# Kernel optimization log

Hardware: AMD Instinct MI355X
Metric: run time of the kernel (lower is better)

Reference implementation:

```python
import math
import jax, jax.numpy as jnp
import numpy as np

BLOCK = 128
QMAX = 7.0            # 2**(4-1) - 1
ALPHA = 2.5139        # optimal Gaussian scale for 4 bits
N_LEVELS = 2 * 7 + 1  # 15
TRUST = ALPHA / N_LEVELS


def _build_hadamard(size: int) -> np.ndarray:
    H = np.ones((1, 1), dtype=np.float64)
    while H.shape[0] < size:
        H = np.block([[H, H], [H, -H]])
    return (H / math.sqrt(size)).astype(np.float32)


def _hadamard_rotate(x, H):
    # blockwise rotation along last dim; H is symmetric orthogonal so this is
    # its own inverse
    *batch, dim = x.shape
    bs = H.shape[0]
    return (x.reshape(*batch, dim // bs, bs) @ H).reshape(*batch, dim)


def setup_inputs() -> dict:
    key = jax.random.key(0)
    x = jax.random.normal(key, (4, 4096, 4096), dtype=jnp.float32)
    H = jnp.asarray(_build_hadamard(BLOCK))
    return {"x": x, "H": H}


def reference(x, H):
    x_h = _hadamard_rotate(x, H)
    # RMS over last dim
    std = jnp.maximum(jnp.sqrt(jnp.mean(x_h * x_h, axis=-1, keepdims=True)), 1e-8)
    step = (ALPHA * std) / QMAX
    xq = jnp.clip(jnp.round(x_h / step), -QMAX, QMAX) * step
    mask = (jnp.abs(xq - x_h) <= std * TRUST).astype(x_h.dtype)
    # straight-through: gradient flows only through x_h * mask
    out_h = x_h * mask + jax.lax.stop_gradient(xq - x_h * mask)
    return _hadamard_rotate(out_h, H)
```

## Files before the change

kernel.cpp:

```cpp
#include <hip/hip_runtime.h>
#include <hip/hip_bf16.h>


#define HTQ_ALPHA 2.5139f
#define HTQ_QMAX  7.0f

template <int CTRL>
__device__ __forceinline__ float dpp_perm(float f) {
    int r = __builtin_amdgcn_update_dpp(__float_as_int(f), __float_as_int(f),
                                        CTRL, 0xF, 0xF, true);
    return __int_as_float(r);
}

template <int MASK>
__device__ __forceinline__ float swz_xor(float f) {
    int r = __builtin_amdgcn_ds_swizzle(__float_as_int(f), (MASK << 10) | 0x1F);
    return __int_as_float(r);
}

#define CROSS_STAGE(GETP, BIT)                                   \
    {                                                            \
        const float sg = (lane & (BIT)) ? -1.0f : 1.0f;          \
        _Pragma("unroll")                                        \
        for (int i = 0; i < 64; ++i) {                           \
            float p = GETP(v[i]);                                \
            v[i] = fmaf(sg, v[i], p);                            \
        }                                                        \
    }

__device__ __forceinline__ void fwht128(float v[64], int lane) {
#pragma unroll
    for (int g = 0; g < 16; ++g) {
        float a0 = v[4 * g], a1 = v[4 * g + 1], a2 = v[4 * g + 2], a3 = v[4 * g + 3];
        float t0 = a0 + a1, t1 = a0 - a1, t2 = a2 + a3, t3 = a2 - a3;
        v[4 * g]     = t0 + t2;
        v[4 * g + 1] = t1 + t3;
        v[4 * g + 2] = t0 - t2;
        v[4 * g + 3] = t1 - t3;
    }
    CROSS_STAGE(dpp_perm<0xB1>, 1)
    CROSS_STAGE(dpp_perm<0x4E>, 2)
    CROSS_STAGE(swz_xor<4>, 4)
    CROSS_STAGE(dpp_perm<0x128>, 8)
    CROSS_STAGE(swz_xor<16>, 16)
}

__global__ __launch_bounds__(256) void htq_kernel(const float* __restrict__ x,
                                                  float* __restrict__ out) {
    const int gid  = blockIdx.x * 256 + threadIdx.x;
    const int row  = gid >> 6;
    const int lane = threadIdx.x & 63;

    const size_t base = (size_t)row * 4096 + (size_t)lane * 4;

    float v[64];
    float4* v4 = reinterpret_cast<float4*>(v);
    const float4* g4 = reinterpret_cast<const float4*>(x + base);
#pragma unroll
    for (int t = 0; t < 16; ++t) v4[t] = g4[(size_t)t * 64];

    fwht128(v, lane);

    float ss = 0.0f;
#pragma unroll
    for (int i = 0; i < 64; ++i) ss = fmaf(v[i], v[i], ss);
#pragma unroll
    for (int m = 1; m < 64; m <<= 1) ss += __shfl_xor(ss, m, 64);

    float std_y = sqrtf(ss * (1.0f / 4096.0f));
    std_y = fmaxf(std_y, 1.1313708499e-7f);
    const float step = (HTQ_ALPHA * std_y) / HTQ_QMAX;

#pragma unroll
    for (int i = 0; i < 64; ++i) {
        float r = rintf(v[i] / step);
        r = fminf(fmaxf(r, -HTQ_QMAX), HTQ_QMAX);
        v[i] = r * step;
    }

    fwht128(v, lane);

    float4* o4 = reinterpret_cast<float4*>(out + base);
#pragma unroll
    for (int t = 0; t < 16; ++t) {
        float4 w = v4[t];
        w.x *= 0.0078125f; w.y *= 0.0078125f; w.z *= 0.0078125f; w.w *= 0.0078125f;
        o4[(size_t)t * 64] = w;
    }
}

extern "C" void kernel_launch(void* const* d_in, const int* in_sizes, int n_in,
                              void* d_out, int out_size, void* d_ws, size_t ws_size,
                              hipStream_t stream) {
    const float* x = (const float*)d_in[0];
    float* out = (float*)d_out;

    const int n    = in_sizes[0];
    const int rows = n / 4096;
    const int blocks = (rows * 64) / 256;

    hipLaunchKernelGGL(htq_kernel, dim3(blocks), dim3(256), 0, stream, x, out);
}
```

Before: 438.9 us.

## Remap lanes so two FWHT stages run in registers, add nontemporal IO

Changes the data layout so each group of 8 lanes owns one 128-element Hadamard block with four 4-element chunks per lane. The last two butterfly stages become in-register adds instead of DPP and swizzle cross-lane exchanges. It also swaps the per-element divide for a reciprocal multiply plus one Newton-style correction, folds the output 1/128 scale into the dequant step, and uses nontemporal loads and stores. Memory coalescing changes: each float4 access now covers 8 lanes times 16 bytes contiguously, per 128-element chunk.

```diff
diff --git a/kernel.cpp b/kernel.cpp
--- a/kernel.cpp
+++ b/kernel.cpp
@@ -1,9 +1,10 @@
 #include <hip/hip_runtime.h>
-#include <hip/hip_bf16.h>
 
 
 #define HTQ_ALPHA 2.5139f
 #define HTQ_QMAX  7.0f
+
+typedef float vfloat4 __attribute__((ext_vector_type(4)));
 
 template <int CTRL>
 __device__ __forceinline__ float dpp_perm(float f) {
@@ -41,8 +42,20 @@
     CROSS_STAGE(dpp_perm<0xB1>, 1)
     CROSS_STAGE(dpp_perm<0x4E>, 2)
     CROSS_STAGE(swz_xor<4>, 4)
-    CROSS_STAGE(dpp_perm<0x128>, 8)
-    CROSS_STAGE(swz_xor<16>, 16)
+#pragma unroll
+    for (int i = 0; i < 64; ++i) {
+        if (i & 4) continue;
+        float a = v[i], b = v[i + 4];
+        v[i] = a + b;
+        v[i + 4] = a - b;
+    }
+#pragma unroll
+    for (int i = 0; i < 64; ++i) {
+        if (i & 8) continue;
+        float a = v[i], b = v[i + 8];
+        v[i] = a + b;
+        v[i + 8] = a - b;
+    }
 }
 
 __global__ __launch_bounds__(256) void htq_kernel(const float* __restrict__ x,
@@ -50,14 +63,17 @@
     const int gid  = blockIdx.x * 256 + threadIdx.x;
     const int row  = gid >> 6;
     const int lane = threadIdx.x & 63;
+    const int oct  = lane >> 3;
+    const int sub  = lane & 7;
 
-    const size_t base = (size_t)row * 4096 + (size_t)lane * 4;
+    const size_t base = (size_t)row * 4096 + (size_t)(oct * 128 + sub * 4);
 
     float v[64];
-    float4* v4 = reinterpret_cast<float4*>(v);
-    const float4* g4 = reinterpret_cast<const float4*>(x + base);
+    vfloat4* v4 = reinterpret_cast<vfloat4*>(v);
+    const vfloat4* g4 = reinterpret_cast<const vfloat4*>(x + base);
 #pragma unroll
-    for (int t = 0; t < 16; ++t) v4[t] = g4[(size_t)t * 64];
+    for (int t = 0; t < 16; ++t)
+        v4[t] = __builtin_nontemporal_load(&g4[(t >> 2) * 256 + (t & 3) * 8]);
 
     fwht128(v, lane);
 
@@ -69,24 +85,27 @@
 
     float std_y = sqrtf(ss * (1.0f / 4096.0f));
     std_y = fmaxf(std_y, 1.1313708499e-7f);
-    const float step = (HTQ_ALPHA * std_y) / HTQ_QMAX;
+    const float step  = (HTQ_ALPHA * std_y) / HTQ_QMAX;
+    const float inv   = 1.0f / step;
+    const float step2 = step * 0.0078125f;
 
 #pragma unroll
     for (int i = 0; i < 64; ++i) {
-        float r = rintf(v[i] / step);
+        const float xv = v[i];
+        float q0 = xv * inv;
+        float rr = fmaf(-q0, step, xv);
+        float q  = fmaf(rr, inv, q0);
+        float r  = rintf(q);
         r = fminf(fmaxf(r, -HTQ_QMAX), HTQ_QMAX);
-        v[i] = r * step;
+        v[i] = r * step2;
     }
 
     fwht128(v, lane);
 
-    float4* o4 = reinterpret_cast<float4*>(out + base);
+    vfloat4* o4 = reinterpret_cast<vfloat4*>(out + base);
 #pragma unroll
-    for (int t = 0; t < 16; ++t) {
-        float4 w = v4[t];
-        w.x *= 0.0078125f; w.y *= 0.0078125f; w.z *= 0.0078125f; w.w *= 0.0078125f;
-        o4[(size_t)t * 64] = w;
-    }
+    for (int t = 0; t < 16; ++t)
+        __builtin_nontemporal_store(v4[t], &o4[(t >> 2) * 256 + (t & 3) * 8]);
 }
 
 extern "C" void kernel_launch(void* const* d_in, const int* in_sizes, int n_in,
```

Measured after the change: 428.0 us. 2.5% less time.
